# Optimization experiments

Measured on AMD Instinct MI355X. Metric: run time of the kernel, lower is better.

Reference implementation:

```python
import jax, jax.numpy as jnp
import numpy as np

B, S, H, I, E, K = 2, 2048, 1024, 2048, 8, 2


def setup_inputs() -> dict:
    key = jax.random.key(0)
    k1, k2, k3, k4, k5 = jax.random.split(key, 5)
    scale_h = 1.0 / np.sqrt(H)
    scale_i = 1.0 / np.sqrt(I)
    return {
        "x": jax.random.normal(k1, (B, S, H), dtype=jnp.float32),
        "Wg": jax.random.normal(k2, (H, E), dtype=jnp.float32) * scale_h,
        "W11": jax.random.normal(k3, (E, H, I), dtype=jnp.float32) * scale_h,
        "W12": jax.random.normal(k4, (E, H, I), dtype=jnp.float32) * scale_h,
        "W2": jax.random.normal(k5, (E, I, H), dtype=jnp.float32) * scale_i,
    }


def reference(x, Wg, W11, W12, W2):
    # Router: softmax over experts, then top-k with renormalization (+1e-8 as in torch ref)
    gate_scores = jax.nn.softmax(x @ Wg, axis=-1)          # [B,S,E]
    topk_scores, topk_idx = jax.lax.top_k(gate_scores, K)   # [B,S,K]
    topk_scores = topk_scores / (topk_scores.sum(-1, keepdims=True) + 1e-8)

    # Dense per-expert SwiGLU on all tokens (matches reference's masked-dense math)
    gate = jnp.einsum('bsh,ehi->bsei', x, W11)              # [B,S,E,I]
    value = jnp.einsum('bsh,ehi->bsei', x, W12)
    fused = (gate * jax.nn.sigmoid(gate)) * value           # SiLU(gate) * value
    expert_out = jnp.einsum('bsei,eih->bseh', fused, W2)    # [B,S,E,H]

    # Gather the top-k experts' outputs per token and combine with routing weights
    gathered = jnp.take_along_axis(expert_out, topk_idx[..., None], axis=2)  # [B,S,K,H]
    out = jnp.sum(topk_scores[..., None] * gathered, axis=2)                 # [B,S,H]
    return out
```

## Files before the change

kernel.cpp:

```cpp
#include <hip/hip_runtime.h>
#include <hip/hip_bf16.h>
#include <stdint.h>

#define B_ 2
#define S_ 2048
#define H_ 1024
#define I_ 2048
#define E_ 8
#define TOK (B_*S_)
#define PAIRS (TOK*2)
#define MAXBLK 80

typedef __bf16 bf16_t;
typedef __bf16 bf16x4 __attribute__((ext_vector_type(4)));
typedef __bf16 bf16x8 __attribute__((ext_vector_type(8)));
typedef float  f32x4  __attribute__((ext_vector_type(4)));
typedef float  f32x16 __attribute__((ext_vector_type(16)));

__device__ __forceinline__ void gl_lds16(const bf16_t* g, bf16_t* l) {
    __builtin_amdgcn_global_load_lds(
        (const __attribute__((address_space(1))) unsigned int*)g,
        (__attribute__((address_space(3))) unsigned int*)l, 16, 0, 0);
}

__global__ void router_kernel(const float* __restrict__ x, const float* __restrict__ Wg,
                              int* __restrict__ top2e, float* __restrict__ top2w,
                              int* __restrict__ counts, bf16_t* __restrict__ xb) {
    int wave = threadIdx.x >> 6;
    int lane = threadIdx.x & 63;
    int t = blockIdx.x * 4 + wave;
    if (t >= TOK) return;
    float acc[E_];
#pragma unroll
    for (int e = 0; e < E_; e++) acc[e] = 0.f;
    const float* xrow = x + (size_t)t * H_;
    for (int j = 0; j < H_ / 64; j++) {
        int h = j * 64 + lane;
        float xv = xrow[h];
        const float4* wg = (const float4*)(Wg + (size_t)h * E_);
        float4 w0 = wg[0], w1 = wg[1];
        acc[0] += xv * w0.x; acc[1] += xv * w0.y; acc[2] += xv * w0.z; acc[3] += xv * w0.w;
        acc[4] += xv * w1.x; acc[5] += xv * w1.y; acc[6] += xv * w1.z; acc[7] += xv * w1.w;
    }
#pragma unroll
    for (int part = 0; part < 2; part++) {
        int idx = part * 512 + lane * 8;
        float4 v0 = *(const float4*)(xrow + idx);
        float4 v1 = *(const float4*)(xrow + idx + 4);
        bf16x8 ov = { (bf16_t)v0.x, (bf16_t)v0.y, (bf16_t)v0.z, (bf16_t)v0.w,
                      (bf16_t)v1.x, (bf16_t)v1.y, (bf16_t)v1.z, (bf16_t)v1.w };
        *(bf16x8*)(xb + (size_t)t * H_ + idx) = ov;
    }
#pragma unroll
    for (int e = 0; e < E_; e++) {
#pragma unroll
        for (int m = 32; m >= 1; m >>= 1) acc[e] += __shfl_xor(acc[e], m, 64);
    }
    if (lane == 0) {
        float mx = acc[0];
        for (int e = 1; e < E_; e++) mx = fmaxf(mx, acc[e]);
        float p[E_]; float z = 0.f;
        for (int e = 0; e < E_; e++) { p[e] = __expf(acc[e] - mx); z += p[e]; }
        for (int e = 0; e < E_; e++) p[e] /= z;
        int i1 = 0; float p1 = p[0];
        for (int e = 1; e < E_; e++) if (p[e] > p1) { p1 = p[e]; i1 = e; }
        int i2 = -1; float p2 = -1.f;
        for (int e = 0; e < E_; e++) if (e != i1 && p[e] > p2) { p2 = p[e]; i2 = e; }
        float s = p1 + p2 + 1e-8f;
        top2e[t * 2]     = i1; top2e[t * 2 + 1] = i2;
        top2w[t * 2]     = p1 / s; top2w[t * 2 + 1] = p2 / s;
        atomicAdd(&counts[i1], 1);
        atomicAdd(&counts[i2], 1);
    }
}

__global__ __launch_bounds__(256) void scanfill_kernel(
    const int* __restrict__ counts, int* __restrict__ offsets,
    int* __restrict__ blk_e, int* __restrict__ blk_m0, int* __restrict__ nblk,
    const int* __restrict__ top2e, int* __restrict__ pair_tok, int* __restrict__ inv) {
    __shared__ int s_cur[E_];
    if (threadIdx.x == 0) {
        int run = 0, b = 0;
        for (int e = 0; e < E_; e++) {
            offsets[e] = run; s_cur[e] = run;
            int c = counts[e];
            for (int m0 = 0; m0 < c; m0 += 128) { blk_e[b] = e; blk_m0[b] = m0; b++; }
            run += c;
        }
        nblk[0] = b;
    }
    __syncthreads();
    for (int p = threadIdx.x; p < PAIRS; p += 256) {
        int e = top2e[p];
        int pos = atomicAdd(&s_cur[e], 1);
        pair_tok[pos] = p >> 1;
        inv[p] = pos;
    }
}

__global__ __launch_bounds__(256) void wtrans_kernel(
    const float* __restrict__ W11, const float* __restrict__ W12,
    const float* __restrict__ W2,
    bf16_t* __restrict__ W11t, bf16_t* __restrict__ W12t, bf16_t* __restrict__ W2t) {
    __shared__ float tile[64][129];
    int z = blockIdx.y;
    int wsel = z >> 3, e = z & 7;
    const float* sbase; bf16_t* dbase; int R, C, tx, ty;
    if (wsel == 0)      { sbase = W11; dbase = W11t; R = H_; C = I_; }
    else if (wsel == 1) { sbase = W12; dbase = W12t; R = H_; C = I_; }
    else                { sbase = W2;  dbase = W2t;  R = I_; C = H_; }
    if (wsel < 2) { tx = blockIdx.x & 15; ty = blockIdx.x >> 4; }
    else          { tx = blockIdx.x & 7;  ty = blockIdx.x >> 3; }
    const float* s = sbase + (size_t)e * R * C;
    bf16_t* d = dbase + (size_t)e * R * C;
    int c0 = tx * 128, r0 = ty * 64;
    int t = threadIdx.x;
#pragma unroll
    for (int j = 0; j < 8; j++) {
        int flat = j * 256 + t;
        int r = flat >> 5;
        int c4 = (flat & 31) * 4;
        float4 v = *(const float4*)(s + (size_t)(r0 + r) * C + c0 + c4);
        tile[r][c4 + 0] = v.x;
        tile[r][c4 + 1] = v.y;
        tile[r][c4 + 2] = v.z;
        tile[r][c4 + 3] = v.w;
    }
    __syncthreads();
#pragma unroll
    for (int j = 0; j < 4; j++) {
        int flat = j * 256 + t;
        int orow = flat >> 3;
        int seg  = (flat & 7) * 8;
        bf16x8 v;
#pragma unroll
        for (int k = 0; k < 8; k++) v[k] = (bf16_t)tile[seg + k][orow];
        *(bf16x8*)(d + (size_t)(c0 + orow) * R + r0 + seg) = v;
    }
}

__global__ __launch_bounds__(256, 2) void gemm1_kernel(
    const bf16_t* __restrict__ xb,
    const bf16_t* __restrict__ W11t,
    const bf16_t* __restrict__ W12t,
    const int* __restrict__ counts, const int* __restrict__ offsets,
    const int* __restrict__ blk_e, const int* __restrict__ blk_m0,
    const int* __restrict__ nblk,
    const int* __restrict__ pair_tok,
    bf16_t* __restrict__ fused)
{
    int by = blockIdx.y;
    if (by >= nblk[0]) return;
    int e = blk_e[by];
    int m0 = blk_m0[by];
    int cnt = counts[e];
    int off = offsets[e];
    int n0 = blockIdx.x * 128;

    __shared__ __align__(16) bf16_t la[128 * 64];
    __shared__ __align__(16) bf16_t lb[256 * 64];

    int tid = threadIdx.x;
    int w = tid >> 6, lane = tid & 63;
    int wm = w >> 1, wn = w & 1;
    int lrow = lane >> 3, lcol = lane & 7;
    int scol = lcol ^ lrow;

    const bf16_t* aptr4[4];
    const bf16_t* bptr[8];
#pragma unroll
    for (int it = 0; it < 4; it++) {
        int r = it * 32 + w * 8 + lrow;
        int grow = m0 + r;
        int tok = pair_tok[off + (grow < cnt ? grow : 0)];
        aptr4[it] = xb + (size_t)tok * H_ + scol * 8;
    }
#pragma unroll
    for (int it = 0; it < 8; it++) {
        int r = it * 32 + w * 8 + lrow;
        const bf16_t* base = (r < 128)
            ? (W11t + ((size_t)e * I_ + n0 + r) * H_)
            : (W12t + ((size_t)e * I_ + n0 + (r - 128)) * H_);
        bptr[it] = base + scol * 8;
    }

    f32x16 acc[2][4];
#pragma unroll
    for (int a = 0; a < 2; a++)
#pragma unroll
        for (int b = 0; b < 4; b++) acc[a][b] = (f32x16)(0.f);

    int r32 = lane & 31;
    int khalf = lane >> 5;
    int rx = r32 & 7;

    for (int k0 = 0; k0 < H_; k0 += 64) {
#pragma unroll
        for (int it = 0; it < 4; it++)
            gl_lds16(aptr4[it] + k0, &la[(it * 32 + w * 8) * 64]);
#pragma unroll
        for (int it = 0; it < 8; it++)
            gl_lds16(bptr[it] + k0, &lb[(it * 32 + w * 8) * 64]);
        __syncthreads();
#pragma unroll
        for (int t16 = 0; t16 < 4; t16++) {
            int seg = t16 * 2 + khalf;
            bf16x8 af[2], bfr[4];
#pragma unroll
            for (int ms = 0; ms < 2; ms++) {
                int row = wm * 64 + ms * 32 + r32;
                af[ms] = *(const bf16x8*)&la[row * 64 + (seg ^ rx) * 8];
            }
#pragma unroll
            for (int ns = 0; ns < 2; ns++) {
                int browg = wn * 64 + ns * 32 + r32;
                bfr[ns]     = *(const bf16x8*)&lb[browg * 64 + (seg ^ rx) * 8];
                bfr[ns + 2] = *(const bf16x8*)&lb[(browg + 128) * 64 + (seg ^ rx) * 8];
            }
#pragma unroll
            for (int ms = 0; ms < 2; ms++)
#pragma unroll
                for (int ns = 0; ns < 4; ns++)
                    acc[ms][ns] = __builtin_amdgcn_mfma_f32_32x32x16_bf16(
                        af[ms], bfr[ns], acc[ms][ns], 0, 0, 0);
        }
        __syncthreads();
    }

#pragma unroll
    for (int ms = 0; ms < 2; ms++) {
#pragma unroll
        for (int ns = 0; ns < 2; ns++) {
            int i = n0 + wn * 64 + ns * 32 + r32;
#pragma unroll
            for (int reg = 0; reg < 16; reg++) {
                int rrow = (reg & 3) + 8 * (reg >> 2) + 4 * khalf;
                int grow = m0 + wm * 64 + ms * 32 + rrow;
                if (grow < cnt) {
                    float g = acc[ms][ns][reg];
                    float v = acc[ms][ns + 2][reg];
                    float f = g * v / (1.f + __expf(-g));
                    fused[(size_t)(off + grow) * I_ + i] = (bf16_t)f;
                }
            }
        }
    }
}

__global__ __launch_bounds__(256, 3) void gemm2_kernel(
    const bf16_t* __restrict__ fused,
    const bf16_t* __restrict__ W2t,
    const int* __restrict__ counts, const int* __restrict__ offsets,
    const int* __restrict__ blk_e, const int* __restrict__ blk_m0,
    const int* __restrict__ nblk,
    bf16_t* __restrict__ y)
{
    int by = blockIdx.y;
    if (by >= nblk[0]) return;
    int e = blk_e[by];
    int m0 = blk_m0[by];
    int cnt = counts[e];
    int off = offsets[e];
    int n0 = blockIdx.x * 128;

    __shared__ __align__(16) bf16_t la[128 * 64];
    __shared__ __align__(16) bf16_t lb[128 * 64];

    int tid = threadIdx.x;
    int w = tid >> 6, lane = tid & 63;
    int wm = w >> 1, wn = w & 1;
    int lrow = lane >> 3, lcol = lane & 7;
    int scol = lcol ^ lrow;

    const bf16_t* aptr[4];
    const bf16_t* bptr[4];
#pragma unroll
    for (int it = 0; it < 4; it++) {
        int r = it * 32 + w * 8 + lrow;
        int grow = m0 + r;
        if (grow >= cnt) grow = cnt - 1;
        aptr[it] = fused + (size_t)(off + grow) * I_ + scol * 8;
        bptr[it] = W2t + ((size_t)e * H_ + n0 + r) * I_ + scol * 8;
    }

    f32x16 acc[2][2];
#pragma unroll
    for (int a = 0; a < 2; a++)
#pragma unroll
        for (int b = 0; b < 2; b++) acc[a][b] = (f32x16)(0.f);

    int r32 = lane & 31;
    int khalf = lane >> 5;
    int rx = r32 & 7;

    for (int k0 = 0; k0 < I_; k0 += 64) {
#pragma unroll
        for (int it = 0; it < 4; it++) {
            gl_lds16(aptr[it] + k0, &la[(it * 32 + w * 8) * 64]);
            gl_lds16(bptr[it] + k0, &lb[(it * 32 + w * 8) * 64]);
        }
        __syncthreads();
#pragma unroll
        for (int t16 = 0; t16 < 4; t16++) {
            int seg = t16 * 2 + khalf;
            bf16x8 af[2], bfr[2];
#pragma unroll
            for (int ms = 0; ms < 2; ms++) {
                int row = wm * 64 + ms * 32 + r32;
                af[ms] = *(const bf16x8*)&la[row * 64 + (seg ^ rx) * 8];
            }
#pragma unroll
            for (int ns = 0; ns < 2; ns++) {
                int brow = wn * 64 + ns * 32 + r32;
                bfr[ns] = *(const bf16x8*)&lb[brow * 64 + (seg ^ rx) * 8];
            }
#pragma unroll
            for (int ms = 0; ms < 2; ms++)
#pragma unroll
                for (int ns = 0; ns < 2; ns++)
                    acc[ms][ns] = __builtin_amdgcn_mfma_f32_32x32x16_bf16(
                        af[ms], bfr[ns], acc[ms][ns], 0, 0, 0);
        }
        __syncthreads();
    }

#pragma unroll
    for (int ms = 0; ms < 2; ms++) {
#pragma unroll
        for (int reg = 0; reg < 16; reg++) {
            int rrow = (reg & 3) + 8 * (reg >> 2) + 4 * khalf;
            int grow = m0 + wm * 64 + ms * 32 + rrow;
            if (grow < cnt) {
                int slot = off + grow;
#pragma unroll
                for (int ns = 0; ns < 2; ns++) {
                    int h = n0 + wn * 64 + ns * 32 + r32;
                    y[(size_t)slot * H_ + h] = (bf16_t)acc[ms][ns][reg];
                }
            }
        }
    }
}

__global__ __launch_bounds__(256) void combine_kernel(
    const bf16_t* __restrict__ y, const int* __restrict__ inv,
    const float* __restrict__ top2w, float* __restrict__ out) {
    int t = blockIdx.x;
    int h = threadIdx.x * 4;
    int s1 = inv[t * 2], s2 = inv[t * 2 + 1];
    float w1 = top2w[t * 2], w2 = top2w[t * 2 + 1];
    bf16x4 a = *(const bf16x4*)(y + (size_t)s1 * H_ + h);
    bf16x4 b = *(const bf16x4*)(y + (size_t)s2 * H_ + h);
    f32x4 r;
#pragma unroll
    for (int k = 0; k < 4; k++) r[k] = w1 * (float)a[k] + w2 * (float)b[k];
    *(f32x4*)(out + (size_t)t * H_ + h) = r;
}

extern "C" void kernel_launch(void* const* d_in, const int* in_sizes, int n_in,
                              void* d_out, int out_size, void* d_ws, size_t ws_size,
                              hipStream_t stream) {
    const float* x   = (const float*)d_in[0];
    const float* Wg  = (const float*)d_in[1];
    const float* W11 = (const float*)d_in[2];
    const float* W12 = (const float*)d_in[3];
    const float* W2  = (const float*)d_in[4];
    float* out = (float*)d_out;

    char* ws = (char*)d_ws;
    size_t o = 0;
    auto alloc = [&](size_t bytes) { size_t r = o; o = (o + bytes + 255) & ~(size_t)255; return r; };
    int*    counts   = (int*)(ws + alloc(E_ * 4));
    int*    offsets  = (int*)(ws + alloc(E_ * 4));
    int*    blk_e    = (int*)(ws + alloc(MAXBLK * 4));
    int*    blk_m0   = (int*)(ws + alloc(MAXBLK * 4));
    int*    nblk     = (int*)(ws + alloc(4));
    int*    top2e    = (int*)(ws + alloc(TOK * 2 * 4));
    float*  top2w    = (float*)(ws + alloc(TOK * 2 * 4));
    int*    pair_tok = (int*)(ws + alloc(PAIRS * 4));
    int*    inv      = (int*)(ws + alloc(TOK * 2 * 4));
    bf16_t* xb       = (bf16_t*)(ws + alloc((size_t)TOK * H_ * 2));
    bf16_t* W11t     = (bf16_t*)(ws + alloc((size_t)E_ * I_ * H_ * 2));
    bf16_t* W12t     = (bf16_t*)(ws + alloc((size_t)E_ * I_ * H_ * 2));
    bf16_t* W2t      = (bf16_t*)(ws + alloc((size_t)E_ * I_ * H_ * 2));
    bf16_t* fusedbuf = (bf16_t*)(ws + alloc((size_t)PAIRS * I_ * 2));
    bf16_t* ybuf     = (bf16_t*)(ws + alloc((size_t)PAIRS * H_ * 2));

    hipMemsetAsync(counts, 0, E_ * 4, stream);

    router_kernel<<<TOK / 4, 256, 0, stream>>>(x, Wg, top2e, top2w, counts, xb);
    scanfill_kernel<<<1, 256, 0, stream>>>(counts, offsets, blk_e, blk_m0, nblk,
                                           top2e, pair_tok, inv);
    wtrans_kernel<<<dim3(256, 24), 256, 0, stream>>>(W11, W12, W2, W11t, W12t, W2t);

    gemm1_kernel<<<dim3(I_ / 128, MAXBLK), 256, 0, stream>>>(
        xb, W11t, W12t, counts, offsets, blk_e, blk_m0, nblk, pair_tok, fusedbuf);
    gemm2_kernel<<<dim3(H_ / 128, MAXBLK), 256, 0, stream>>>(
        fusedbuf, W2t, counts, offsets, blk_e, blk_m0, nblk, ybuf);
    combine_kernel<<<TOK, 256, 0, stream>>>(ybuf, inv, top2w, out);
}
```

Measured before the change: 492.8 us.

## Double-buffer LDS with 256-row tiles and 8 waves in MoE GEMMs

```diff
diff --git a/kernel.cpp b/kernel.cpp
--- a/kernel.cpp
+++ b/kernel.cpp
@@ -9,7 +9,7 @@
 #define E_ 8
 #define TOK (B_*S_)
 #define PAIRS (TOK*2)
-#define MAXBLK 80
+#define MAXBLK 40
 
 typedef __bf16 bf16_t;
 typedef __bf16 bf16x4 __attribute__((ext_vector_type(4)));
@@ -84,7 +84,7 @@
         for (int e = 0; e < E_; e++) {
             offsets[e] = run; s_cur[e] = run;
             int c = counts[e];
-            for (int m0 = 0; m0 < c; m0 += 128) { blk_e[b] = e; blk_m0[b] = m0; b++; }
+            for (int m0 = 0; m0 < c; m0 += 256) { blk_e[b] = e; blk_m0[b] = m0; b++; }
             run += c;
         }
         nblk[0] = b;
@@ -139,7 +139,9 @@
     }
 }
 
-__global__ __launch_bounds__(256, 2) void gemm1_kernel(
+#define G1_LDSE ((256 + 256) * 64)
+
+__global__ __launch_bounds__(512, 2) void gemm1_kernel(
     const bf16_t* __restrict__ xb,
     const bf16_t* __restrict__ W11t,
     const bf16_t* __restrict__ W12t,
@@ -157,97 +159,109 @@
     int off = offsets[e];
     int n0 = blockIdx.x * 128;
 
-    __shared__ __align__(16) bf16_t la[128 * 64];
-    __shared__ __align__(16) bf16_t lb[256 * 64];
+    extern __shared__ __align__(16) bf16_t smem[];
 
     int tid = threadIdx.x;
     int w = tid >> 6, lane = tid & 63;
-    int wm = w >> 1, wn = w & 1;
+    int wm = w >> 2, wn = w & 3;
     int lrow = lane >> 3, lcol = lane & 7;
     int scol = lcol ^ lrow;
-
-    const bf16_t* aptr4[4];
-    const bf16_t* bptr[8];
+    int r32 = lane & 31, khalf = lane >> 5, rx = r32 & 7;
+    int rbase = w * 8 + lrow;
+
+    const bf16_t* aptr[4];
+    const bf16_t* bptr[4];
 #pragma unroll
     for (int it = 0; it < 4; it++) {
-        int r = it * 32 + w * 8 + lrow;
-        int grow = m0 + r;
+        int arow = it * 64 + rbase;
+        int grow = m0 + arow;
         int tok = pair_tok[off + (grow < cnt ? grow : 0)];
-        aptr4[it] = xb + (size_t)tok * H_ + scol * 8;
-    }
-#pragma unroll
-    for (int it = 0; it < 8; it++) {
-        int r = it * 32 + w * 8 + lrow;
-        const bf16_t* base = (r < 128)
-            ? (W11t + ((size_t)e * I_ + n0 + r) * H_)
-            : (W12t + ((size_t)e * I_ + n0 + (r - 128)) * H_);
-        bptr[it] = base + scol * 8;
-    }
-
-    f32x16 acc[2][4];
-#pragma unroll
-    for (int a = 0; a < 2; a++)
-#pragma unroll
-        for (int b = 0; b < 4; b++) acc[a][b] = (f32x16)(0.f);
-
-    int r32 = lane & 31;
-    int khalf = lane >> 5;
-    int rx = r32 & 7;
-
-    for (int k0 = 0; k0 < H_; k0 += 64) {
-#pragma unroll
-        for (int it = 0; it < 4; it++)
-            gl_lds16(aptr4[it] + k0, &la[(it * 32 + w * 8) * 64]);
-#pragma unroll
-        for (int it = 0; it < 8; it++)
-            gl_lds16(bptr[it] + k0, &lb[(it * 32 + w * 8) * 64]);
-        __syncthreads();
-#pragma unroll
-        for (int t16 = 0; t16 < 4; t16++) {
-            int seg = t16 * 2 + khalf;
-            bf16x8 af[2], bfr[4];
-#pragma unroll
-            for (int ms = 0; ms < 2; ms++) {
-                int row = wm * 64 + ms * 32 + r32;
-                af[ms] = *(const bf16x8*)&la[row * 64 + (seg ^ rx) * 8];
+        aptr[it] = xb + (size_t)tok * H_ + scol * 8;
+        int wrow = n0 + it * 32 + (rbase & 31);
+        const bf16_t* wb = (rbase < 32) ? W11t : W12t;
+        bptr[it] = wb + ((size_t)e * I_ + wrow) * H_ + scol * 8;
+    }
+
+    f32x16 accg[4], accv[4];
+#pragma unroll
+    for (int m = 0; m < 4; m++) { accg[m] = (f32x16)(0.f); accv[m] = (f32x16)(0.f); }
+
+    {
+        bf16_t* An = smem;
+        bf16_t* Bn = smem + 256 * 64;
+#pragma unroll
+        for (int it = 0; it < 4; it++) gl_lds16(aptr[it], &An[(it * 64 + w * 8) * 64]);
+#pragma unroll
+        for (int it = 0; it < 4; it++) gl_lds16(bptr[it], &Bn[(it * 64 + w * 8) * 64]);
+    }
+
+    const int NT = H_ / 64;
+    for (int t = 0; t < NT; t++) {
+        bf16_t* Ac = smem + (t & 1) * G1_LDSE;
+        bf16_t* Bc = Ac + 256 * 64;
+        if (t + 1 < NT) {
+            bf16_t* An = smem + ((t + 1) & 1) * G1_LDSE;
+            bf16_t* Bn = An + 256 * 64;
+            int ko = (t + 1) * 64;
+#pragma unroll
+            for (int it = 0; it < 4; it++) gl_lds16(aptr[it] + ko, &An[(it * 64 + w * 8) * 64]);
+#pragma unroll
+            for (int it = 0; it < 4; it++) gl_lds16(bptr[it] + ko, &Bn[(it * 64 + w * 8) * 64]);
+            asm volatile("s_waitcnt vmcnt(8)" ::: "memory");
+        } else {
+            asm volatile("s_waitcnt vmcnt(0)" ::: "memory");
+        }
+        __builtin_amdgcn_s_barrier();
+#pragma unroll
+        for (int p = 0; p < 4; p++) {
+            int slot = p * 2 + khalf;
+            bf16x8 af[4], bfr[2];
+#pragma unroll
+            for (int ms = 0; ms < 4; ms++) {
+                int row = wm * 128 + ms * 32 + r32;
+                af[ms] = *(const bf16x8*)&Ac[row * 64 + ((slot ^ rx)) * 8];
             }
-#pragma unroll
-            for (int ns = 0; ns < 2; ns++) {
-                int browg = wn * 64 + ns * 32 + r32;
-                bfr[ns]     = *(const bf16x8*)&lb[browg * 64 + (seg ^ rx) * 8];
-                bfr[ns + 2] = *(const bf16x8*)&lb[(browg + 128) * 64 + (seg ^ rx) * 8];
+            {
+                int rg = wn * 64 + r32;
+                bfr[0] = *(const bf16x8*)&Bc[rg * 64 + (slot ^ rx) * 8];
+                bfr[1] = *(const bf16x8*)&Bc[(rg + 32) * 64 + (slot ^ rx) * 8];
             }
-#pragma unroll
-            for (int ms = 0; ms < 2; ms++)
-#pragma unroll
-                for (int ns = 0; ns < 4; ns++)
-                    acc[ms][ns] = __builtin_amdgcn_mfma_f32_32x32x16_bf16(
-                        af[ms], bfr[ns], acc[ms][ns], 0, 0, 0);
-        }
-        __syncthreads();
-    }
-
-#pragma unroll
-    for (int ms = 0; ms < 2; ms++) {
-#pragma unroll
-        for (int ns = 0; ns < 2; ns++) {
-            int i = n0 + wn * 64 + ns * 32 + r32;
-#pragma unroll
-            for (int reg = 0; reg < 16; reg++) {
-                int rrow = (reg & 3) + 8 * (reg >> 2) + 4 * khalf;
-                int grow = m0 + wm * 64 + ms * 32 + rrow;
-                if (grow < cnt) {
-                    float g = acc[ms][ns][reg];
-                    float v = acc[ms][ns + 2][reg];
-                    float f = g * v / (1.f + __expf(-g));
-                    fused[(size_t)(off + grow) * I_ + i] = (bf16_t)f;
-                }
+            __builtin_amdgcn_s_barrier();
+            asm volatile("s_waitcnt lgkmcnt(0)" ::: "memory");
+            __builtin_amdgcn_sched_barrier(0);
+            __builtin_amdgcn_s_setprio(1);
+#pragma unroll
+            for (int ms = 0; ms < 4; ms++)
+                accg[ms] = __builtin_amdgcn_mfma_f32_32x32x16_bf16(af[ms], bfr[0], accg[ms], 0, 0, 0);
+#pragma unroll
+            for (int ms = 0; ms < 4; ms++)
+                accv[ms] = __builtin_amdgcn_mfma_f32_32x32x16_bf16(af[ms], bfr[1], accv[ms], 0, 0, 0);
+            __builtin_amdgcn_s_setprio(0);
+            __builtin_amdgcn_sched_barrier(0);
+            __builtin_amdgcn_s_barrier();
+        }
+    }
+
+    int i = n0 + wn * 32 + r32;
+#pragma unroll
+    for (int ms = 0; ms < 4; ms++) {
+#pragma unroll
+        for (int reg = 0; reg < 16; reg++) {
+            int rrow = (reg & 3) + 8 * (reg >> 2) + 4 * khalf;
+            int grow = m0 + wm * 128 + ms * 32 + rrow;
+            if (grow < cnt) {
+                float g = accg[ms][reg];
+                float v = accv[ms][reg];
+                float f = g * v / (1.f + __expf(-g));
+                fused[(size_t)(off + grow) * I_ + i] = (bf16_t)f;
             }
         }
     }
 }
 
-__global__ __launch_bounds__(256, 3) void gemm2_kernel(
+#define G2_LDSE ((256 + 128) * 64)
+
+__global__ __launch_bounds__(512, 2) void gemm2_kernel(
     const bf16_t* __restrict__ fused,
     const bf16_t* __restrict__ W2t,
     const int* __restrict__ counts, const int* __restrict__ offsets,
@@ -263,24 +277,28 @@
     int off = offsets[e];
     int n0 = blockIdx.x * 128;
 
-    __shared__ __align__(16) bf16_t la[128 * 64];
-    __shared__ __align__(16) bf16_t lb[128 * 64];
+    extern __shared__ __align__(16) bf16_t smem[];
 
     int tid = threadIdx.x;
     int w = tid >> 6, lane = tid & 63;
     int wm = w >> 1, wn = w & 1;
     int lrow = lane >> 3, lcol = lane & 7;
     int scol = lcol ^ lrow;
+    int r32 = lane & 31, khalf = lane >> 5, rx = r32 & 7;
+    int rbase = w * 8 + lrow;
 
     const bf16_t* aptr[4];
-    const bf16_t* bptr[4];
+    const bf16_t* bptr[2];
 #pragma unroll
     for (int it = 0; it < 4; it++) {
-        int r = it * 32 + w * 8 + lrow;
-        int grow = m0 + r;
+        int grow = m0 + it * 64 + rbase;
         if (grow >= cnt) grow = cnt - 1;
         aptr[it] = fused + (size_t)(off + grow) * I_ + scol * 8;
-        bptr[it] = W2t + ((size_t)e * H_ + n0 + r) * I_ + scol * 8;
+    }
+#pragma unroll
+    for (int it = 0; it < 2; it++) {
+        int row = it * 64 + rbase;
+        bptr[it] = W2t + ((size_t)e * H_ + n0 + row) * I_ + scol * 8;
     }
 
     f32x16 acc[2][2];
@@ -289,39 +307,65 @@
 #pragma unroll
         for (int b = 0; b < 2; b++) acc[a][b] = (f32x16)(0.f);
 
-    int r32 = lane & 31;
-    int khalf = lane >> 5;
-    int rx = r32 & 7;
-
-    for (int k0 = 0; k0 < I_; k0 += 64) {
-#pragma unroll
-        for (int it = 0; it < 4; it++) {
-            gl_lds16(aptr[it] + k0, &la[(it * 32 + w * 8) * 64]);
-            gl_lds16(bptr[it] + k0, &lb[(it * 32 + w * 8) * 64]);
-        }
-        __syncthreads();
-#pragma unroll
-        for (int t16 = 0; t16 < 4; t16++) {
-            int seg = t16 * 2 + khalf;
-            bf16x8 af[2], bfr[2];
-#pragma unroll
-            for (int ms = 0; ms < 2; ms++) {
-                int row = wm * 64 + ms * 32 + r32;
-                af[ms] = *(const bf16x8*)&la[row * 64 + (seg ^ rx) * 8];
+    {
+        bf16_t* An = smem;
+        bf16_t* Bn = smem + 256 * 64;
+#pragma unroll
+        for (int it = 0; it < 4; it++) gl_lds16(aptr[it], &An[(it * 64 + w * 8) * 64]);
+#pragma unroll
+        for (int it = 0; it < 2; it++) gl_lds16(bptr[it], &Bn[(it * 64 + w * 8) * 64]);
+    }
+
+    const int NT = I_ / 64;
+    for (int t = 0; t < NT; t++) {
+        bf16_t* Ac = smem + (t & 1) * G2_LDSE;
+        bf16_t* Bc = Ac + 256 * 64;
+        if (t + 1 < NT) {
+            bf16_t* An = smem + ((t + 1) & 1) * G2_LDSE;
+            bf16_t* Bn = An + 256 * 64;
+            int ko = (t + 1) * 64;
+#pragma unroll
+            for (int it = 0; it < 4; it++) gl_lds16(aptr[it] + ko, &An[(it * 64 + w * 8) * 64]);
+#pragma unroll
+            for (int it = 0; it < 2; it++) gl_lds16(bptr[it] + ko, &Bn[(it * 64 + w * 8) * 64]);
+            asm volatile("s_waitcnt vmcnt(6)" ::: "memory");
+        } else {
+            asm volatile("s_waitcnt vmcnt(0)" ::: "memory");
+        }
+        __builtin_amdgcn_s_barrier();
+#pragma unroll
+        for (int p2 = 0; p2 < 2; p2++) {
+            bf16x8 af[2][2], bfr[2][2];
+#pragma unroll
+            for (int sub = 0; sub < 2; sub++) {
+                int slot = p2 * 4 + sub * 2 + khalf;
+#pragma unroll
+                for (int ms = 0; ms < 2; ms++) {
+                    int row = wm * 64 + ms * 32 + r32;
+                    af[sub][ms] = *(const bf16x8*)&Ac[row * 64 + (slot ^ rx) * 8];
+                }
+#pragma unroll
+                for (int ns = 0; ns < 2; ns++) {
+                    int row = wn * 64 + ns * 32 + r32;
+                    bfr[sub][ns] = *(const bf16x8*)&Bc[row * 64 + (slot ^ rx) * 8];
+                }
             }
-#pragma unroll
-            for (int ns = 0; ns < 2; ns++) {
-                int brow = wn * 64 + ns * 32 + r32;
-                bfr[ns] = *(const bf16x8*)&lb[brow * 64 + (seg ^ rx) * 8];
-            }
-#pragma unroll
-            for (int ms = 0; ms < 2; ms++)
-#pragma unroll
-                for (int ns = 0; ns < 2; ns++)
-                    acc[ms][ns] = __builtin_amdgcn_mfma_f32_32x32x16_bf16(
-                        af[ms], bfr[ns], acc[ms][ns], 0, 0, 0);
-        }
-        __syncthreads();
+            __builtin_amdgcn_s_barrier();
+            asm volatile("s_waitcnt lgkmcnt(0)" ::: "memory");
+            __builtin_amdgcn_sched_barrier(0);
+            __builtin_amdgcn_s_setprio(1);
+#pragma unroll
+            for (int sub = 0; sub < 2; sub++)
+#pragma unroll
+                for (int ms = 0; ms < 2; ms++)
+#pragma unroll
+                    for (int ns = 0; ns < 2; ns++)
+                        acc[ms][ns] = __builtin_amdgcn_mfma_f32_32x32x16_bf16(
+                            af[sub][ms], bfr[sub][ns], acc[ms][ns], 0, 0, 0);
+            __builtin_amdgcn_s_setprio(0);
+            __builtin_amdgcn_sched_barrier(0);
+            __builtin_amdgcn_s_barrier();
+        }
     }
 
 #pragma unroll
@@ -386,6 +430,15 @@
     bf16_t* fusedbuf = (bf16_t*)(ws + alloc((size_t)PAIRS * I_ * 2));
     bf16_t* ybuf     = (bf16_t*)(ws + alloc((size_t)PAIRS * H_ * 2));
 
+    static bool attr_set = false;
+    if (!attr_set) {
+        hipFuncSetAttribute((const void*)gemm1_kernel,
+                            hipFuncAttributeMaxDynamicSharedMemorySize, 2 * G1_LDSE * 2);
+        hipFuncSetAttribute((const void*)gemm2_kernel,
+                            hipFuncAttributeMaxDynamicSharedMemorySize, 2 * G2_LDSE * 2);
+        attr_set = true;
+    }
+
     hipMemsetAsync(counts, 0, E_ * 4, stream);
 
     router_kernel<<<TOK / 4, 256, 0, stream>>>(x, Wg, top2e, top2w, counts, xb);
@@ -393,9 +446,9 @@
                                            top2e, pair_tok, inv);
     wtrans_kernel<<<dim3(256, 24), 256, 0, stream>>>(W11, W12, W2, W11t, W12t, W2t);
 
-    gemm1_kernel<<<dim3(I_ / 128, MAXBLK), 256, 0, stream>>>(
+    gemm1_kernel<<<dim3(I_ / 128, MAXBLK), 512, 2 * G1_LDSE * 2, stream>>>(
         xb, W11t, W12t, counts, offsets, blk_e, blk_m0, nblk, pair_tok, fusedbuf);
-    gemm2_kernel<<<dim3(H_ / 128, MAXBLK), 256, 0, stream>>>(
+    gemm2_kernel<<<dim3(H_ / 128, MAXBLK), 512, 2 * G2_LDSE * 2, stream>>>(
         fusedbuf, W2t, counts, offsets, blk_e, blk_m0, nblk, ybuf);
     combine_kernel<<<TOK, 256, 0, stream>>>(ybuf, inv, top2w, out);
 }
```

After: 534.3 us. +8.4%, slower.

## Double-buffer LDS tiles with K=32 stages in both expert GEMMs

Applied to the files above, without the earlier changes.

```diff
diff --git a/kernel.cpp b/kernel.cpp
--- a/kernel.cpp
+++ b/kernel.cpp
@@ -22,6 +22,8 @@
         (const __attribute__((address_space(1))) unsigned int*)g,
         (__attribute__((address_space(3))) unsigned int*)l, 16, 0, 0);
 }
+
+__device__ __forceinline__ void cfence() { asm volatile("" ::: "memory"); }
 
 __global__ void router_kernel(const float* __restrict__ x, const float* __restrict__ Wg,
                               int* __restrict__ top2e, float* __restrict__ top2w,
@@ -157,31 +159,33 @@
     int off = offsets[e];
     int n0 = blockIdx.x * 128;
 
-    __shared__ __align__(16) bf16_t la[128 * 64];
-    __shared__ __align__(16) bf16_t lb[256 * 64];
+    __shared__ __align__(16) bf16_t la[2][128 * 32];
+    __shared__ __align__(16) bf16_t lb[2][256 * 32];
 
     int tid = threadIdx.x;
     int w = tid >> 6, lane = tid & 63;
     int wm = w >> 1, wn = w & 1;
-    int lrow = lane >> 3, lcol = lane & 7;
-    int scol = lcol ^ lrow;
-
-    const bf16_t* aptr4[4];
-    const bf16_t* bptr[8];
-#pragma unroll
-    for (int it = 0; it < 4; it++) {
-        int r = it * 32 + w * 8 + lrow;
+    int lrow4 = lane >> 2;
+    int lcol4 = lane & 3;
+    int sch   = lcol4 ^ (lrow4 & 3);
+    int r32 = lane & 31, khalf = lane >> 5;
+
+    const bf16_t* aptr[2];
+    const bf16_t* bptr[4];
+#pragma unroll
+    for (int it = 0; it < 2; it++) {
+        int r = it * 64 + w * 16 + lrow4;
         int grow = m0 + r;
         int tok = pair_tok[off + (grow < cnt ? grow : 0)];
-        aptr4[it] = xb + (size_t)tok * H_ + scol * 8;
-    }
-#pragma unroll
-    for (int it = 0; it < 8; it++) {
-        int r = it * 32 + w * 8 + lrow;
+        aptr[it] = xb + (size_t)tok * H_ + sch * 8;
+    }
+#pragma unroll
+    for (int it = 0; it < 4; it++) {
+        int r = it * 64 + w * 16 + lrow4;
         const bf16_t* base = (r < 128)
             ? (W11t + ((size_t)e * I_ + n0 + r) * H_)
             : (W12t + ((size_t)e * I_ + n0 + (r - 128)) * H_);
-        bptr[it] = base + scol * 8;
+        bptr[it] = base + sch * 8;
     }
 
     f32x16 acc[2][4];
@@ -190,32 +194,45 @@
 #pragma unroll
         for (int b = 0; b < 4; b++) acc[a][b] = (f32x16)(0.f);
 
-    int r32 = lane & 31;
-    int khalf = lane >> 5;
-    int rx = r32 & 7;
-
-    for (int k0 = 0; k0 < H_; k0 += 64) {
-#pragma unroll
-        for (int it = 0; it < 4; it++)
-            gl_lds16(aptr4[it] + k0, &la[(it * 32 + w * 8) * 64]);
-#pragma unroll
-        for (int it = 0; it < 8; it++)
-            gl_lds16(bptr[it] + k0, &lb[(it * 32 + w * 8) * 64]);
-        __syncthreads();
-#pragma unroll
-        for (int t16 = 0; t16 < 4; t16++) {
+#pragma unroll
+    for (int it = 0; it < 2; it++) gl_lds16(aptr[it], &la[0][(it * 64 + w * 16) * 32]);
+#pragma unroll
+    for (int it = 0; it < 4; it++) gl_lds16(bptr[it], &lb[0][(it * 64 + w * 16) * 32]);
+
+    const int NT = H_ / 32;
+    for (int t = 0; t < NT; t++) {
+        int cur = t & 1;
+        if (t + 1 < NT) {
+            int nxt = cur ^ 1;
+            int ko = (t + 1) * 32;
+#pragma unroll
+            for (int it = 0; it < 2; it++) gl_lds16(aptr[it] + ko, &la[nxt][(it * 64 + w * 16) * 32]);
+#pragma unroll
+            for (int it = 0; it < 4; it++) gl_lds16(bptr[it] + ko, &lb[nxt][(it * 64 + w * 16) * 32]);
+            asm volatile("s_waitcnt vmcnt(6)" ::: "memory");
+        } else {
+            asm volatile("s_waitcnt vmcnt(0)" ::: "memory");
+        }
+        __builtin_amdgcn_s_barrier();
+        __builtin_amdgcn_sched_barrier(0);
+        cfence();
+
+        const bf16_t* A = la[cur];
+        const bf16_t* Bb = lb[cur];
+#pragma unroll
+        for (int t16 = 0; t16 < 2; t16++) {
             int seg = t16 * 2 + khalf;
             bf16x8 af[2], bfr[4];
 #pragma unroll
             for (int ms = 0; ms < 2; ms++) {
                 int row = wm * 64 + ms * 32 + r32;
-                af[ms] = *(const bf16x8*)&la[row * 64 + (seg ^ rx) * 8];
+                af[ms] = *(const bf16x8*)&A[row * 32 + (seg ^ (r32 & 3)) * 8];
             }
 #pragma unroll
             for (int ns = 0; ns < 2; ns++) {
                 int browg = wn * 64 + ns * 32 + r32;
-                bfr[ns]     = *(const bf16x8*)&lb[browg * 64 + (seg ^ rx) * 8];
-                bfr[ns + 2] = *(const bf16x8*)&lb[(browg + 128) * 64 + (seg ^ rx) * 8];
+                bfr[ns]     = *(const bf16x8*)&Bb[browg * 32 + (seg ^ (r32 & 3)) * 8];
+                bfr[ns + 2] = *(const bf16x8*)&Bb[(browg + 128) * 32 + (seg ^ (r32 & 3)) * 8];
             }
 #pragma unroll
             for (int ms = 0; ms < 2; ms++)
@@ -224,7 +241,10 @@
                     acc[ms][ns] = __builtin_amdgcn_mfma_f32_32x32x16_bf16(
                         af[ms], bfr[ns], acc[ms][ns], 0, 0, 0);
         }
-        __syncthreads();
+        asm volatile("s_waitcnt lgkmcnt(0)" ::: "memory");
+        __builtin_amdgcn_sched_barrier(0);
+        __builtin_amdgcn_s_barrier();
+        cfence();
     }
 
 #pragma unroll
@@ -263,24 +283,26 @@
     int off = offsets[e];
     int n0 = blockIdx.x * 128;
 
-    __shared__ __align__(16) bf16_t la[128 * 64];
-    __shared__ __align__(16) bf16_t lb[128 * 64];
+    __shared__ __align__(16) bf16_t la[2][128 * 32];
+    __shared__ __align__(16) bf16_t lb[2][128 * 32];
 
     int tid = threadIdx.x;
     int w = tid >> 6, lane = tid & 63;
     int wm = w >> 1, wn = w & 1;
-    int lrow = lane >> 3, lcol = lane & 7;
-    int scol = lcol ^ lrow;
-
-    const bf16_t* aptr[4];
-    const bf16_t* bptr[4];
-#pragma unroll
-    for (int it = 0; it < 4; it++) {
-        int r = it * 32 + w * 8 + lrow;
+    int lrow4 = lane >> 2;
+    int lcol4 = lane & 3;
+    int sch   = lcol4 ^ (lrow4 & 3);
+    int r32 = lane & 31, khalf = lane >> 5;
+
+    const bf16_t* aptr[2];
+    const bf16_t* bptr[2];
+#pragma unroll
+    for (int it = 0; it < 2; it++) {
+        int r = it * 64 + w * 16 + lrow4;
         int grow = m0 + r;
         if (grow >= cnt) grow = cnt - 1;
-        aptr[it] = fused + (size_t)(off + grow) * I_ + scol * 8;
-        bptr[it] = W2t + ((size_t)e * H_ + n0 + r) * I_ + scol * 8;
+        aptr[it] = fused + (size_t)(off + grow) * I_ + sch * 8;
+        bptr[it] = W2t + ((size_t)e * H_ + n0 + r) * I_ + sch * 8;
     }
 
     f32x16 acc[2][2];
@@ -289,30 +311,46 @@
 #pragma unroll
         for (int b = 0; b < 2; b++) acc[a][b] = (f32x16)(0.f);
 
-    int r32 = lane & 31;
-    int khalf = lane >> 5;
-    int rx = r32 & 7;
-
-    for (int k0 = 0; k0 < I_; k0 += 64) {
-#pragma unroll
-        for (int it = 0; it < 4; it++) {
-            gl_lds16(aptr[it] + k0, &la[(it * 32 + w * 8) * 64]);
-            gl_lds16(bptr[it] + k0, &lb[(it * 32 + w * 8) * 64]);
-        }
-        __syncthreads();
-#pragma unroll
-        for (int t16 = 0; t16 < 4; t16++) {
+#pragma unroll
+    for (int it = 0; it < 2; it++) {
+        gl_lds16(aptr[it], &la[0][(it * 64 + w * 16) * 32]);
+        gl_lds16(bptr[it], &lb[0][(it * 64 + w * 16) * 32]);
+    }
+
+    const int NT = I_ / 32;
+    for (int t = 0; t < NT; t++) {
+        int cur = t & 1;
+        if (t + 1 < NT) {
+            int nxt = cur ^ 1;
+            int ko = (t + 1) * 32;
+#pragma unroll
+            for (int it = 0; it < 2; it++) {
+                gl_lds16(aptr[it] + ko, &la[nxt][(it * 64 + w * 16) * 32]);
+                gl_lds16(bptr[it] + ko, &lb[nxt][(it * 64 + w * 16) * 32]);
+            }
+            asm volatile("s_waitcnt vmcnt(4)" ::: "memory");
+        } else {
+            asm volatile("s_waitcnt vmcnt(0)" ::: "memory");
+        }
+        __builtin_amdgcn_s_barrier();
+        __builtin_amdgcn_sched_barrier(0);
+        cfence();
+
+        const bf16_t* A = la[cur];
+        const bf16_t* Bb = lb[cur];
+#pragma unroll
+        for (int t16 = 0; t16 < 2; t16++) {
             int seg = t16 * 2 + khalf;
             bf16x8 af[2], bfr[2];
 #pragma unroll
             for (int ms = 0; ms < 2; ms++) {
                 int row = wm * 64 + ms * 32 + r32;
-                af[ms] = *(const bf16x8*)&la[row * 64 + (seg ^ rx) * 8];
+                af[ms] = *(const bf16x8*)&A[row * 32 + (seg ^ (r32 & 3)) * 8];
             }
 #pragma unroll
             for (int ns = 0; ns < 2; ns++) {
                 int brow = wn * 64 + ns * 32 + r32;
-                bfr[ns] = *(const bf16x8*)&lb[brow * 64 + (seg ^ rx) * 8];
+                bfr[ns] = *(const bf16x8*)&Bb[brow * 32 + (seg ^ (r32 & 3)) * 8];
             }
 #pragma unroll
             for (int ms = 0; ms < 2; ms++)
@@ -321,7 +359,10 @@
                     acc[ms][ns] = __builtin_amdgcn_mfma_f32_32x32x16_bf16(
                         af[ms], bfr[ns], acc[ms][ns], 0, 0, 0);
         }
-        __syncthreads();
+        asm volatile("s_waitcnt lgkmcnt(0)" ::: "memory");
+        __builtin_amdgcn_sched_barrier(0);
+        __builtin_amdgcn_s_barrier();
+        cfence();
     }
 
 #pragma unroll
```

Measured after the change: 537.6 us. +9.1%, slower.
